# Kernel optimization log

Measured on AMD Instinct MI355X. Metric: run time of the kernel, lower is better.

Reference implementation:

```python
import jax, jax.numpy as jnp
import numpy as np

ADAPTER_RATIO = 0.2


def setup_inputs() -> dict:
    key = jax.random.key(0)
    k1, k2, k3, k4, k5 = jax.random.split(key, 5)
    B, D, R, N_DOM, N_TXT = 16384, 1024, 256, 3, 1380
    image_features = jax.random.normal(k1, (B, D), dtype=jnp.float32)
    domain_labels = jax.random.randint(k2, (B,), 0, N_DOM, dtype=jnp.int64)
    W1 = jax.random.normal(k3, (N_DOM, D, R), dtype=jnp.float32) * 0.02
    W2 = jax.random.normal(k4, (N_DOM, R, D), dtype=jnp.float32) * 0.02
    txt = jax.random.normal(k5, (N_TXT, D), dtype=jnp.float32)
    # text features are L2-normalized at module init (encode_text then norm)
    text_features = txt / jnp.linalg.norm(txt, axis=-1, keepdims=True)
    logit_scale = jnp.asarray(np.log(1.0 / 0.07), dtype=jnp.float32)  # CLIP init
    return {
        "image_features": image_features,
        "domain_labels": domain_labels,
        "W1": W1,
        "W2": W2,
        "text_features": text_features,
        "logit_scale": logit_scale,
    }


def reference(image_features, domain_labels, W1, W2, text_features, logit_scale):
    # Domain-routed adapter MLP: run all n_domains experts (n is tiny), then
    # select the routed output per sample (equivalent to the per-sample loop).
    h = jax.nn.relu(jnp.einsum("bd,ndr->bnr", image_features, W1))  # [B,n,R]
    a = jax.nn.relu(jnp.einsum("bnr,nrd->bnd", h, W2))              # [B,n,D]
    idx = domain_labels[:, None, None]                                # [B,1,1]
    adapter_features = jnp.take_along_axis(a, idx, axis=1)[:, 0, :]   # [B,D]
    fused = ADAPTER_RATIO * adapter_features + (1.0 - ADAPTER_RATIO) * image_features
    fused = fused / jnp.linalg.norm(fused, axis=-1, keepdims=True)
    # text_features already normalized; concat over domains done upstream: [N_TXT, D]
    logits = jnp.exp(logit_scale) * (fused @ text_features.T)         # [B, N_TXT]
    return logits
```

## Files before the change

### kernel.cpp

```cpp
#include <hip/hip_runtime.h>
#include <hip/hip_bf16.h>
#include <math.h>

using bf16 = __hip_bfloat16;
typedef __attribute__((ext_vector_type(8))) short bf16x8;
typedef __attribute__((ext_vector_type(4))) float f32x4;
typedef __attribute__((ext_vector_type(4))) unsigned short us4;

#define GAS __attribute__((address_space(1)))
#define LAS __attribute__((address_space(3)))

__device__ __forceinline__ void gload_lds16(const bf16* g, bf16* lds) {
  __builtin_amdgcn_global_load_lds((const GAS void*)g, (LAS void*)lds, 16, 0, 0);
}
__device__ __forceinline__ float b2f(unsigned short u) {
  union { unsigned short s; bf16 b; } x; x.s = u; return __bfloat162float(x.b);
}

__global__ __launch_bounds__(256) void hist_k(const int* __restrict__ lab,
                                              int* __restrict__ blockHist) {
  const int blk = blockIdx.x, t = threadIdx.x;
  const int lane = t & 63, w = t >> 6;
  const int d = lab[blk * 256 + t];
  __shared__ int wc[4][3];
#pragma unroll
  for (int dd = 0; dd < 3; ++dd) {
    unsigned long long m = __ballot(d == dd);
    if (lane == 0) wc[w][dd] = __popcll(m);
  }
  __syncthreads();
  if (t < 3) blockHist[blk * 3 + t] = wc[0][t] + wc[1][t] + wc[2][t] + wc[3][t];
}

__global__ __launch_bounds__(256) void scan_k(const int* __restrict__ blockHist,
                                              int* __restrict__ blockOff,
                                              int* __restrict__ meta) {
  __shared__ int h[64][3];
  __shared__ int tot[3];
  const int t = threadIdx.x;
  if (t < 192) h[t / 3][t % 3] = blockHist[t];
  __syncthreads();
  if (t < 3) {
    int s = 0;
    for (int b = 0; b < 64; ++b) { int v = h[b][t]; h[b][t] = s; s += v; }
    tot[t] = s;
    meta[t] = s;
  }
  __syncthreads();
  if (t == 0) { meta[4] = 0; meta[5] = tot[0]; meta[6] = tot[0] + tot[1]; }
  if (t < 192) {
    int b = t / 3, d = t % 3;
    int base = (d == 0) ? 0 : (d == 1 ? tot[0] : tot[0] + tot[1]);
    blockOff[t] = base + h[b][d];
  }
}

__global__ __launch_bounds__(256) void scatter2_k(const int* __restrict__ lab,
                                                  const int* __restrict__ blockOff,
                                                  int* __restrict__ perm,
                                                  int* __restrict__ iperm) {
  const int blk = blockIdx.x, t = threadIdx.x;
  const int lane = t & 63, w = t >> 6;
  const int i = blk * 256 + t;
  const int d = lab[i];
  __shared__ int wc[4][3];
  unsigned long long mymask = 0;
#pragma unroll
  for (int dd = 0; dd < 3; ++dd) {
    unsigned long long m = __ballot(d == dd);
    if (lane == 0) wc[w][dd] = __popcll(m);
    if (dd == d) mymask = m;
  }
  __syncthreads();
  int woff = 0;
  for (int ww = 0; ww < w; ++ww) woff += wc[ww][d];
  const unsigned long long lt = ((unsigned long long)1 << lane) - 1;
  const int rank = blockOff[blk * 3 + d] + woff + __popcll(mymask & lt);
  perm[rank] = i;
  iperm[i] = rank;
}

__global__ __launch_bounds__(256) void prep_k(const float* __restrict__ x,
                                              const float* __restrict__ txt,
                                              const float* __restrict__ W1,
                                              const float* __restrict__ W2,
                                              const int* __restrict__ iperm,
                                              bf16* __restrict__ Xbc,
                                              bf16* __restrict__ Tb,
                                              bf16* __restrict__ W1T,
                                              bf16* __restrict__ W2T) {
  __shared__ float s[64][65];
  if (blockIdx.x < 384) {
    int b = blockIdx.x;
    const float* W; bf16* WT; int R, C;
    if (b < 192) { W = W1; WT = W1T; R = 1024; C = 256; }
    else         { b -= 192; W = W2; WT = W2T; R = 256; C = 1024; }
    const int d = b / 64, tb = b % 64;
    const int tilesPerRow = C / 64;
    const int r0 = (tb / tilesPerRow) * 64;
    const int c0 = (tb % tilesPerRow) * 64;
    const float* Wd = W + (size_t)d * R * C;
    bf16* WTd = WT + (size_t)d * R * C;
    const int tx = threadIdx.x & 63, ty = threadIdx.x >> 6;
#pragma unroll
    for (int i = 0; i < 16; ++i)
      s[ty + i * 4][tx] = Wd[(size_t)(r0 + ty + i * 4) * C + c0 + tx];
    __syncthreads();
#pragma unroll
    for (int i = 0; i < 16; ++i)
      WTd[(size_t)(c0 + ty + i * 4) * R + r0 + tx] = __float2bfloat16(s[tx][ty + i * 4]);
    return;
  }
  const int nx = 16384 * 1024 / 4;
  const int ntext = 1536 * 1024;
  const int total = nx + ntext;
  for (int i = (blockIdx.x - 384) * 256 + threadIdx.x; i < total; i += 2048 * 256) {
    if (i < nx) {
      const int row = i >> 8, c4 = i & 255;
      float4 v = ((const float4*)x)[i];
      bf16 t[4] = {__float2bfloat16(v.x), __float2bfloat16(v.y),
                   __float2bfloat16(v.z), __float2bfloat16(v.w)};
      ((us4*)Xbc)[(size_t)iperm[row] * 256 + c4] = *(const us4*)t;
    } else {
      int jj = i - nx;
      Tb[jj] = (jj < 1380 * 1024) ? __float2bfloat16(txt[jj]) : __float2bfloat16(0.f);
    }
  }
}

template <int EPI, int NBLK, int BK>
__global__ __launch_bounds__(256) void gemm_bt(
    const bf16* __restrict__ A, const bf16* __restrict__ BT, bf16* __restrict__ Cv,
    const int* __restrict__ meta, int N, int K, int ldc, int Nvalid,
    const bf16* __restrict__ xb, float* __restrict__ ssp) {
  const int bid = blockIdx.x;
  const int xcd = bid & 7;
  const int seq = bid >> 3;
  const int nblkidx = seq % NBLK;
  const int dm = xcd + 8 * (seq / NBLK);
  const int dom = dm >> 7;
  const int mblk = dm & 127;

  const int cnt = meta[dom];
  const int base = meta[4 + dom];
  BT += (size_t)dom * N * K;

  const int m0 = mblk * 128;
  if (m0 >= cnt) return;
  const int n0 = nblkidx * 128;

  constexpr int CH = BK / 8;
  __shared__ bf16 sA[2][128][BK];
  __shared__ bf16 sB[2][128][BK];

  const int tid = threadIdx.x;
  const int wid = tid >> 6;
  const int lane = tid & 63;
  const int fr = lane & 15;
  const int fq = lane >> 4;

  auto stage = [&](int buf, int kt) {
    const int koff = kt * BK;
#pragma unroll
    for (int L = 0; L < CH / 2; ++L) {
      const int idx = L * 256 + tid;
      const int r = idx / CH, c = idx % CH;
      int ar = m0 + r; if (ar > cnt - 1) ar = cnt - 1;
      gload_lds16(A + (size_t)(base + ar) * K + koff + ((c ^ (r & (CH - 1))) << 3),
                  &sA[buf][0][0] + ((idx & ~63) << 3));
    }
#pragma unroll
    for (int L = 0; L < CH / 2; ++L) {
      const int idx = L * 256 + tid;
      const int r = idx / CH, c = idx % CH;
      gload_lds16(BT + (size_t)(n0 + r) * K + koff + ((c ^ (r & (CH - 1))) << 3),
                  &sB[buf][0][0] + ((idx & ~63) << 3));
    }
  };

  f32x4 acc[4][4];
#pragma unroll
  for (int m = 0; m < 4; ++m)
#pragma unroll
    for (int n = 0; n < 4; ++n) acc[m][n] = (f32x4){0.f, 0.f, 0.f, 0.f};

  const int nk = K / BK;
  stage(0, 0);
  __syncthreads();
  const int wr = wid >> 1, wc = wid & 1;
  for (int kt = 0; kt < nk; ++kt) {
    const int cur = kt & 1;
    if (kt + 1 < nk) stage(cur ^ 1, kt + 1);
#pragma unroll
    for (int kk = 0; kk < BK / 32; ++kk) {
      const int rchunk = (((kk << 2) + fq) ^ (fr & (CH - 1))) << 3;
      bf16x8 af[4], bfr[4];
#pragma unroll
      for (int m = 0; m < 4; ++m)
        af[m] = *(const bf16x8*)&sA[cur][wr * 64 + m * 16 + fr][0 + rchunk];
#pragma unroll
      for (int n = 0; n < 4; ++n)
        bfr[n] = *(const bf16x8*)&sB[cur][wc * 64 + n * 16 + fr][0 + rchunk];
#pragma unroll
      for (int m = 0; m < 4; ++m)
#pragma unroll
        for (int n = 0; n < 4; ++n)
          acc[m][n] = __builtin_amdgcn_mfma_f32_16x16x32_bf16(af[m], bfr[n], acc[m][n], 0, 0, 0);
    }
    __syncthreads();
  }

  if (EPI == 0) {
#pragma unroll
    for (int m = 0; m < 4; ++m) {
#pragma unroll
      for (int r = 0; r < 4; ++r) {
        const int p = m0 + wr * 64 + m * 16 + fq * 4 + r;
        if (p < cnt) {
          const size_t crow = (size_t)(base + p);
#pragma unroll
          for (int n = 0; n < 4; ++n) {
            const int col = n0 + wc * 64 + n * 16 + fr;
            if (col < Nvalid)
              Cv[crow * (size_t)ldc + col] = __float2bfloat16(fmaxf(acc[m][n][r], 0.f));
          }
        }
      }
    }
  } else {
    __shared__ float ssred[128][2];
#pragma unroll
    for (int m = 0; m < 4; ++m) {
#pragma unroll
      for (int r = 0; r < 4; ++r) {
        const int lr = wr * 64 + m * 16 + fq * 4 + r;
        const int p = m0 + lr;
        float rowss = 0.f;
        if (p < cnt) {
          const size_t crow = (size_t)(base + p);
#pragma unroll
          for (int n = 0; n < 4; ++n) {
            const int col = n0 + wc * 64 + n * 16 + fr;
            const float g = 0.2f * fmaxf(acc[m][n][r], 0.f) +
                            0.8f * b2f(*(const unsigned short*)&xb[crow * 1024 + col]);
            Cv[crow * (size_t)ldc + col] = __float2bfloat16(g);
            rowss += g * g;
          }
        }
        rowss += __shfl_xor(rowss, 1, 16);
        rowss += __shfl_xor(rowss, 2, 16);
        rowss += __shfl_xor(rowss, 4, 16);
        rowss += __shfl_xor(rowss, 8, 16);
        if (fr == 0) ssred[lr][wc] = rowss;
      }
    }
    __syncthreads();
    if (tid < 128) {
      const int p = m0 + tid;
      if (p < cnt)
        ssp[(size_t)nblkidx * 16384 + base + p] = ssred[tid][0] + ssred[tid][1];
    }
  }
}

__global__ __launch_bounds__(256, 2) void gemm3_cnt(
    const bf16* __restrict__ A, const bf16* __restrict__ BT,
    float* __restrict__ C, const float* __restrict__ scale_ptr,
    const float* __restrict__ ssp, const int* __restrict__ perm) {
  extern __shared__ bf16 smem[];
  bf16* sA0 = smem;
  bf16* sB0 = smem + 16384;

  const int tid = threadIdx.x;
  const int lane = tid & 63, wid = tid >> 6;
  const int wr = wid >> 1, wc = wid & 1;
  const int fr = lane & 15, fq = lane >> 4;

  const int bid = blockIdx.x;
  const int x = bid & 7, seq = bid >> 3;
  const int mb = x * 16 + (seq >> 3), nb = seq & 7;
  const int m0 = mb << 7, n0 = nb * 192;

  auto STAGE = [&](int t) {
    const int s = t & 1, koff = t << 6;
    bf16* da = sA0 + (s << 13);
#pragma unroll
    for (int L = 0; L < 4; ++L) {
      const int idx = (L << 8) + tid;
      const int r = idx >> 3, c = idx & 7;
      gload_lds16(A + (size_t)(m0 + r) * 1024 + koff + ((c ^ (r & 7)) << 3),
                  da + ((idx & ~63) << 3));
    }
    bf16* db = sB0 + s * 12288;
#pragma unroll
    for (int L = 0; L < 6; ++L) {
      const int idx = (L << 8) + tid;
      const int r = idx >> 3, c = idx & 7;
      gload_lds16(BT + (size_t)(n0 + r) * 1024 + koff + ((c ^ (r & 7)) << 3),
                  db + ((idx & ~63) << 3));
    }
  };
  auto LDA = [&](int s, int kk, bf16x8* dst) {
    const bf16* base = sA0 + (s << 13);
#pragma unroll
    for (int m = 0; m < 4; ++m) {
      const int row = (wr << 6) + (m << 4) + fr;
      dst[m] = *(const bf16x8*)(base + (row << 6) + ((((kk << 2) + fq) ^ (fr & 7)) << 3));
    }
  };
  auto LDB = [&](int s, int kk, bf16x8* dst) {
    const bf16* base = sB0 + s * 12288;
#pragma unroll
    for (int n = 0; n < 6; ++n) {
      const int row = wc * 96 + (n << 4) + fr;
      dst[n] = *(const bf16x8*)(base + (row << 6) + ((((kk << 2) + fq) ^ (fr & 7)) << 3));
    }
  };

  f32x4 acc[4][6];
#pragma unroll
  for (int m = 0; m < 4; ++m)
#pragma unroll
    for (int n = 0; n < 6; ++n) acc[m][n] = (f32x4){0.f, 0.f, 0.f, 0.f};

  STAGE(0); STAGE(1);
  asm volatile("s_waitcnt vmcnt(10)" ::: "memory");
  __builtin_amdgcn_s_barrier();

  const int nt = 16;
  for (int t = 0; t < nt; ++t) {
    const int s = t & 1;
    bf16x8 a0[4], a1[4], b0[6], b1[6];
    LDA(s, 0, a0); LDB(s, 0, b0);
    LDA(s, 1, a1); LDB(s, 1, b1);
    asm volatile("s_waitcnt lgkmcnt(0)" ::: "memory");
    __builtin_amdgcn_sched_barrier(0);
    __builtin_amdgcn_s_barrier();
    __builtin_amdgcn_sched_barrier(0);
    if (t + 2 < nt) STAGE(t + 2);
    __builtin_amdgcn_s_setprio(1);
#pragma unroll
    for (int m = 0; m < 4; ++m)
#pragma unroll
      for (int n = 0; n < 6; ++n)
        acc[m][n] = __builtin_amdgcn_mfma_f32_16x16x32_bf16(a0[m], b0[n], acc[m][n], 0, 0, 0);
#pragma unroll
    for (int m = 0; m < 4; ++m)
#pragma unroll
      for (int n = 0; n < 6; ++n)
        acc[m][n] = __builtin_amdgcn_mfma_f32_16x16x32_bf16(a1[m], b1[n], acc[m][n], 0, 0, 0);
    __builtin_amdgcn_s_setprio(0);
    if (t + 2 < nt) {
      asm volatile("s_waitcnt vmcnt(10)" ::: "memory");
    } else if (t + 1 < nt) {
      asm volatile("s_waitcnt vmcnt(0)" ::: "memory");
    }
    __builtin_amdgcn_sched_barrier(0);
    __builtin_amdgcn_s_barrier();
    __builtin_amdgcn_sched_barrier(0);
  }

  float* rlds = (float*)smem;
  int*   plds = (int*)((char*)smem + 512);
  if (tid < 128) {
    float s = 0.f;
#pragma unroll
    for (int b = 0; b < 8; ++b) s += ssp[b * 16384 + m0 + tid];
    rlds[tid] = rsqrtf(s);
    plds[tid] = perm[m0 + tid];
  }
  __syncthreads();

  const float sc = expf(*scale_ptr);
#pragma unroll
  for (int m = 0; m < 4; ++m) {
    const int lrow = (wr << 6) + (m << 4) + (fq << 2);
#pragma unroll
    for (int r = 0; r < 4; ++r) {
      const float rv = sc * rlds[lrow + r];
      const size_t orow = (size_t)plds[lrow + r];
#pragma unroll
      for (int n = 0; n < 6; ++n) {
        const int gcol = n0 + wc * 96 + (n << 4) + fr;
        if (gcol < 1380) C[orow * 1380 + gcol] = acc[m][n][r] * rv;
      }
    }
  }
}

extern "C" void kernel_launch(void* const* d_in, const int* in_sizes, int n_in,
                              void* d_out, int out_size, void* d_ws, size_t ws_size,
                              hipStream_t stream) {
  (void)in_sizes; (void)n_in; (void)out_size; (void)ws_size;
  const float* x    = (const float*)d_in[0];
  const int*   lab  = (const int*)d_in[1];
  const float* W1   = (const float*)d_in[2];
  const float* W2   = (const float*)d_in[3];
  const float* text = (const float*)d_in[4];
  const float* lsc  = (const float*)d_in[5];
  float* out = (float*)d_out;

  const int B = 16384, D = 1024, R = 256, NTP = 1536;

  char* p = (char*)d_ws;
  auto carve = [&](size_t bytes) {
    char* r = p;
    p += (bytes + 255) & ~(size_t)255;
    return r;
  };
  int*   meta  = (int*)carve(64);
  int*   bhist = (int*)carve(64 * 3 * 4);
  int*   boff  = (int*)carve(64 * 3 * 4);
  int*   perm  = (int*)carve((size_t)B * 4);
  int*   iperm = (int*)carve((size_t)B * 4);
  float* ssp   = (float*)carve((size_t)8 * B * 4);
  bf16*  Xbc   = (bf16*)carve((size_t)B * D * 2);
  bf16*  W1T   = (bf16*)carve((size_t)3 * R * D * 2);
  bf16*  W2T   = (bf16*)carve((size_t)3 * D * R * 2);
  bf16*  Tb    = (bf16*)carve((size_t)NTP * D * 2);
  bf16*  H     = (bf16*)carve((size_t)B * R * 2);
  bf16*  Fbc   = (bf16*)carve((size_t)B * D * 2);

  hist_k<<<B / 256, 256, 0, stream>>>(lab, bhist);
  scan_k<<<1, 256, 0, stream>>>(bhist, boff, meta);
  scatter2_k<<<B / 256, 256, 0, stream>>>(lab, boff, perm, iperm);

  prep_k<<<384 + 2048, 256, 0, stream>>>(x, text, W1, W2, iperm, Xbc, Tb, W1T, W2T);

  gemm_bt<0, 2, 64><<<768, 256, 0, stream>>>(
      Xbc, W1T, H, meta, R, D, R, R, nullptr, nullptr);
  gemm_bt<1, 8, 64><<<3072, 256, 0, stream>>>(
      H, W2T, Fbc, meta, D, R, D, D, Xbc, ssp);
  gemm3_cnt<<<1024, 256, 81920, stream>>>(Fbc, Tb, out, lsc, ssp, perm);
}
```

Before: 152.1 us.

## Enlarge final GEMM tile to 256x192 with 8 waves and 8-phase interleaved schedule

The logits GEMM now uses 512-thread blocks computing 256x192 tiles, so 512 blocks replace 1024 and each block reuses the text-feature tile across twice as many rows. The main loop is split into four MFMA phases with barriers, interleaving LDS fragment loads and the next-stage global-to-LDS copies for A and B between them. This aims to hide memory latency and cut redundant B traffic. In exchange it uses more LDS per block (112 KiB), adds barriers, and at two blocks per CU may limit occupancy.

Measured after the change: 157.4 us. 1.03x slower.

```diff
diff --git a/kernel.cpp b/kernel.cpp
--- a/kernel.cpp
+++ b/kernel.cpp
@@ -263,106 +263,123 @@
   }
 }
 
-__global__ __launch_bounds__(256, 2) void gemm3_cnt(
+__global__ __launch_bounds__(512, 2) void gemm3_8ph(
     const bf16* __restrict__ A, const bf16* __restrict__ BT,
     float* __restrict__ C, const float* __restrict__ scale_ptr,
     const float* __restrict__ ssp, const int* __restrict__ perm) {
   extern __shared__ bf16 smem[];
   bf16* sA0 = smem;
-  bf16* sB0 = smem + 16384;
+  bf16* sB0 = smem + 32768;
 
   const int tid = threadIdx.x;
   const int lane = tid & 63, wid = tid >> 6;
-  const int wr = wid >> 1, wc = wid & 1;
+  const int wr = wid >> 2, wc = wid & 3;
   const int fr = lane & 15, fq = lane >> 4;
 
   const int bid = blockIdx.x;
   const int x = bid & 7, seq = bid >> 3;
-  const int mb = x * 16 + (seq >> 3), nb = seq & 7;
-  const int m0 = mb << 7, n0 = nb * 192;
-
-  auto STAGE = [&](int t) {
+  const int mb = x * 8 + (seq >> 3), nb = seq & 7;
+  const int m0 = mb << 8, n0 = nb * 192;
+
+  auto STAGE_A = [&](int t) {
     const int s = t & 1, koff = t << 6;
-    bf16* da = sA0 + (s << 13);
+    bf16* da = sA0 + (s << 14);
 #pragma unroll
     for (int L = 0; L < 4; ++L) {
-      const int idx = (L << 8) + tid;
+      const int idx = (L << 9) + tid;
       const int r = idx >> 3, c = idx & 7;
       gload_lds16(A + (size_t)(m0 + r) * 1024 + koff + ((c ^ (r & 7)) << 3),
                   da + ((idx & ~63) << 3));
     }
+  };
+  auto STAGE_B = [&](int t) {
+    const int s = t & 1, koff = t << 6;
     bf16* db = sB0 + s * 12288;
 #pragma unroll
-    for (int L = 0; L < 6; ++L) {
-      const int idx = (L << 8) + tid;
+    for (int L = 0; L < 3; ++L) {
+      const int idx = (L << 9) + tid;
       const int r = idx >> 3, c = idx & 7;
       gload_lds16(BT + (size_t)(n0 + r) * 1024 + koff + ((c ^ (r & 7)) << 3),
                   db + ((idx & ~63) << 3));
     }
   };
-  auto LDA = [&](int s, int kk, bf16x8* dst) {
-    const bf16* base = sA0 + (s << 13);
+  auto LDA4 = [&](int s, int kk, int mh, bf16x8* dst) {
+    const bf16* base = sA0 + (s << 14);
 #pragma unroll
     for (int m = 0; m < 4; ++m) {
-      const int row = (wr << 6) + (m << 4) + fr;
+      const int row = (wr << 7) + (mh << 6) + (m << 4) + fr;
       dst[m] = *(const bf16x8*)(base + (row << 6) + ((((kk << 2) + fq) ^ (fr & 7)) << 3));
     }
   };
-  auto LDB = [&](int s, int kk, bf16x8* dst) {
+  auto LDB3 = [&](int s, int kk, bf16x8* dst) {
     const bf16* base = sB0 + s * 12288;
 #pragma unroll
-    for (int n = 0; n < 6; ++n) {
-      const int row = wc * 96 + (n << 4) + fr;
+    for (int n = 0; n < 3; ++n) {
+      const int row = wc * 48 + (n << 4) + fr;
       dst[n] = *(const bf16x8*)(base + (row << 6) + ((((kk << 2) + fq) ^ (fr & 7)) << 3));
     }
   };
 
-  f32x4 acc[4][6];
-#pragma unroll
-  for (int m = 0; m < 4; ++m)
-#pragma unroll
-    for (int n = 0; n < 6; ++n) acc[m][n] = (f32x4){0.f, 0.f, 0.f, 0.f};
-
-  STAGE(0); STAGE(1);
-  asm volatile("s_waitcnt vmcnt(10)" ::: "memory");
-  __builtin_amdgcn_s_barrier();
+  f32x4 acc[8][3];
+#pragma unroll
+  for (int m = 0; m < 8; ++m)
+#pragma unroll
+    for (int n = 0; n < 3; ++n) acc[m][n] = (f32x4){0.f, 0.f, 0.f, 0.f};
+
+#define SB __builtin_amdgcn_sched_barrier(0)
+#define BAR __builtin_amdgcn_s_barrier()
+#define MM12(AF, BF, MB)                                                          \
+  _Pragma("unroll") for (int m = 0; m < 4; ++m) {                                 \
+    _Pragma("unroll") for (int n = 0; n < 3; ++n) {                               \
+      acc[MB + m][n] = __builtin_amdgcn_mfma_f32_16x16x32_bf16(                   \
+          AF[m], BF[n], acc[MB + m][n], 0, 0, 0);                                 \
+    }                                                                             \
+  }
+
+  STAGE_A(0); STAGE_B(0); STAGE_A(1); STAGE_B(1);
+  asm volatile("s_waitcnt vmcnt(7)" ::: "memory");
+  SB; BAR; SB;
 
   const int nt = 16;
   for (int t = 0; t < nt; ++t) {
     const int s = t & 1;
-    bf16x8 a0[4], a1[4], b0[6], b1[6];
-    LDA(s, 0, a0); LDB(s, 0, b0);
-    LDA(s, 1, a1); LDB(s, 1, b1);
+    bf16x8 a0l[4], a0h[4], a1l[4], a1h[4], b0[3], b1[3];
+    LDA4(s, 0, 0, a0l); LDA4(s, 0, 1, a0h); LDB3(s, 0, b0);
     asm volatile("s_waitcnt lgkmcnt(0)" ::: "memory");
-    __builtin_amdgcn_sched_barrier(0);
-    __builtin_amdgcn_s_barrier();
-    __builtin_amdgcn_sched_barrier(0);
-    if (t + 2 < nt) STAGE(t + 2);
+    SB; BAR; SB;
     __builtin_amdgcn_s_setprio(1);
-#pragma unroll
-    for (int m = 0; m < 4; ++m)
-#pragma unroll
-      for (int n = 0; n < 6; ++n)
-        acc[m][n] = __builtin_amdgcn_mfma_f32_16x16x32_bf16(a0[m], b0[n], acc[m][n], 0, 0, 0);
-#pragma unroll
-    for (int m = 0; m < 4; ++m)
-#pragma unroll
-      for (int n = 0; n < 6; ++n)
-        acc[m][n] = __builtin_amdgcn_mfma_f32_16x16x32_bf16(a1[m], b1[n], acc[m][n], 0, 0, 0);
+    MM12(a0l, b0, 0);
+    __builtin_amdgcn_s_setprio(0);
+    LDA4(s, 1, 0, a1l); LDA4(s, 1, 1, a1h); LDB3(s, 1, b1);
+    asm volatile("s_waitcnt lgkmcnt(0)" ::: "memory");
+    SB; BAR; SB;
+    __builtin_amdgcn_s_setprio(1);
+    MM12(a0h, b0, 4);
+    __builtin_amdgcn_s_setprio(0);
+    if (t + 2 < nt) STAGE_A(t + 2);
+    SB; BAR; SB;
+    __builtin_amdgcn_s_setprio(1);
+    MM12(a1l, b1, 0);
+    __builtin_amdgcn_s_setprio(0);
+    if (t + 2 < nt) STAGE_B(t + 2);
+    SB; BAR; SB;
+    __builtin_amdgcn_s_setprio(1);
+    MM12(a1h, b1, 4);
     __builtin_amdgcn_s_setprio(0);
     if (t + 2 < nt) {
-      asm volatile("s_waitcnt vmcnt(10)" ::: "memory");
+      asm volatile("s_waitcnt vmcnt(7)" ::: "memory");
     } else if (t + 1 < nt) {
       asm volatile("s_waitcnt vmcnt(0)" ::: "memory");
     }
-    __builtin_amdgcn_sched_barrier(0);
-    __builtin_amdgcn_s_barrier();
-    __builtin_amdgcn_sched_barrier(0);
-  }
+    SB; BAR; SB;
+  }
+#undef MM12
+#undef BAR
+#undef SB
 
   float* rlds = (float*)smem;
-  int*   plds = (int*)((char*)smem + 512);
-  if (tid < 128) {
+  int*   plds = (int*)((char*)smem + 1024);
+  if (tid < 256) {
     float s = 0.f;
 #pragma unroll
     for (int b = 0; b < 8; ++b) s += ssp[b * 16384 + m0 + tid];
@@ -373,15 +390,15 @@
 
   const float sc = expf(*scale_ptr);
 #pragma unroll
-  for (int m = 0; m < 4; ++m) {
-    const int lrow = (wr << 6) + (m << 4) + (fq << 2);
+  for (int m = 0; m < 8; ++m) {
+    const int lrow = (wr << 7) + (m << 4) + (fq << 2);
 #pragma unroll
     for (int r = 0; r < 4; ++r) {
       const float rv = sc * rlds[lrow + r];
       const size_t orow = (size_t)plds[lrow + r];
 #pragma unroll
-      for (int n = 0; n < 6; ++n) {
-        const int gcol = n0 + wc * 96 + (n << 4) + fr;
+      for (int n = 0; n < 3; ++n) {
+        const int gcol = n0 + wc * 48 + (n << 4) + fr;
         if (gcol < 1380) C[orow * 1380 + gcol] = acc[m][n][r] * rv;
       }
     }
@@ -431,5 +448,5 @@
       Xbc, W1T, H, meta, R, D, R, R, nullptr, nullptr);
   gemm_bt<1, 8, 64><<<3072, 256, 0, stream>>>(
       H, W2T, Fbc, meta, D, R, D, D, Xbc, ssp);
-  gemm3_cnt<<<1024, 256, 81920, stream>>>(Fbc, Tb, out, lsc, ssp, perm);
-}
+  gemm3_8ph<<<512, 512, 114688, stream>>>(Fbc, Tb, out, lsc, ssp, perm);
+}
```
